# Kernel optimization log

Hardware: AMD Instinct MI355X
Metric: run time of the kernel (lower is better)

Reference implementation:

```python
import jax, jax.numpy as jnp
import numpy as np

LEAK = 0.1
LOG_2PI = float(np.log(2.0 * np.pi))


def setup_inputs() -> dict:
    key = jax.random.key(0)
    k1, k2, k3, k4 = jax.random.split(key, 4)
    B, S, K = 128, 8192, 16
    obvs = jax.random.normal(k1, (B, S, 1), dtype=jnp.float32)
    mu = jax.random.normal(k2, (K,), dtype=jnp.float32)
    log_sigma = 0.1 * jax.random.normal(k3, (K,), dtype=jnp.float32)
    prior_logits = jax.random.normal(k4, (K,), dtype=jnp.float32)
    return {"obvs": obvs, "mu": mu, "log_sigma": log_sigma, "prior_logits": prior_logits}


def _log_transition(num_states: int) -> jnp.ndarray:
    # LeakyTransfer: diagonal-dominant stochastic matrix, stay prob 1-leak,
    # leak mass spread uniformly over the other K-1 states.
    eye = jnp.eye(num_states, dtype=jnp.float32)
    A = (1.0 - LEAK) * eye + (LEAK / (num_states - 1)) * (1.0 - eye)
    return jnp.log(A)


def reference(obvs, mu, log_sigma, prior_logits):
    K = mu.shape[0]
    # Gaussian emission NLL per state: [B, S, K]
    sigma = jnp.exp(log_sigma)
    nll = 0.5 * ((obvs - mu) / sigma) ** 2 + log_sigma + 0.5 * LOG_2PI
    ln_em = -nll  # ln_emission_probs

    log_prior = jax.nn.log_softmax(prior_logits)  # CategoricalPrior
    logA = _log_transition(K)  # [K, K] (from -> to)

    # forward recursion: carry[b, j] = ln_em[b, t, j] + logsumexp_i(carry[b, i] + logA[i, j])
    init = ln_em[:, 0, :] + log_prior  # [B, K]
    em_rest = jnp.swapaxes(ln_em[:, 1:, :], 0, 1)  # [S-1, B, K]

    def step(carry, em_t):
        trans = jax.nn.logsumexp(carry[:, :, None] + logA[None, :, :], axis=1)  # [B, K]
        carry = em_t + trans
        return carry, None

    final, _ = jax.lax.scan(step, init, em_rest)
    return jnp.sum(jax.nn.logsumexp(final, axis=-1))
```

## Files before the change

### kernel.cpp

```cpp
#include <hip/hip_runtime.h>

#define NB 128
#define NS 8192
#define NC 128
#define NCP 8
#define NL (NS / NC)
#define M4 (NL / 4)

#define LOG2E 1.4426950408889634f
#define HLOG2PI 0.918938533204672742f
#define LN2 0.69314718055994531f

#define ROWS 20
#define UNIT 640
#define SLOT 320

typedef float v2f __attribute__((ext_vector_type(2)));

__device__ __forceinline__ float fexp2(float x) { return __builtin_amdgcn_exp2f(x); }
__device__ __forceinline__ float flog2(float x) { return __builtin_amdgcn_logf(x); }

__device__ __forceinline__ float gsum16(float v) {
    v += __shfl_xor(v, 1, 16);
    v += __shfl_xor(v, 2, 16);
    v += __shfl_xor(v, 4, 16);
    v += __shfl_xor(v, 8, 16);
    return v;
}
__device__ __forceinline__ float gmax16(float v) {
    v = fmaxf(v, __shfl_xor(v, 1, 16));
    v = fmaxf(v, __shfl_xor(v, 2, 16));
    v = fmaxf(v, __shfl_xor(v, 4, 16));
    v = fmaxf(v, __shfl_xor(v, 8, 16));
    return v;
}

template <int K>
__device__ __forceinline__ int rotk(int x) {
    return __builtin_amdgcn_mov_dpp(x, 0x120 + K, 0xF, 0xF, true);
}

__device__ __forceinline__ float step2(v2f (&Wv)[8], float T, float xx,
                                       float A2, float B2, float C2) {
    const float amb = 0.9f - 0.1f / 15.0f;
    const float bco = 0.1f / 15.0f;
    float myl = fexp2(fmaf(xx, fmaf(xx, A2, B2), C2));
    int mi = __float_as_int(myl);
    float bT = bco * T;
    v2f bT2 = {bT, bT};
    v2f amb2 = {amb, amb};
    v2f L0 = {myl,                          __int_as_float(rotk<1>(mi))};
    v2f L1 = {__int_as_float(rotk<2>(mi)),  __int_as_float(rotk<3>(mi))};
    v2f L2 = {__int_as_float(rotk<4>(mi)),  __int_as_float(rotk<5>(mi))};
    v2f L3 = {__int_as_float(rotk<6>(mi)),  __int_as_float(rotk<7>(mi))};
    v2f L4 = {__int_as_float(rotk<8>(mi)),  __int_as_float(rotk<9>(mi))};
    v2f L5 = {__int_as_float(rotk<10>(mi)), __int_as_float(rotk<11>(mi))};
    v2f L6 = {__int_as_float(rotk<12>(mi)), __int_as_float(rotk<13>(mi))};
    v2f L7 = {__int_as_float(rotk<14>(mi)), __int_as_float(rotk<15>(mi))};
    Wv[0] = __builtin_elementwise_fma(amb2, Wv[0], bT2) * L0;
    Wv[1] = __builtin_elementwise_fma(amb2, Wv[1], bT2) * L1;
    Wv[2] = __builtin_elementwise_fma(amb2, Wv[2], bT2) * L2;
    Wv[3] = __builtin_elementwise_fma(amb2, Wv[3], bT2) * L3;
    Wv[4] = __builtin_elementwise_fma(amb2, Wv[4], bT2) * L4;
    Wv[5] = __builtin_elementwise_fma(amb2, Wv[5], bT2) * L5;
    Wv[6] = __builtin_elementwise_fma(amb2, Wv[6], bT2) * L6;
    Wv[7] = __builtin_elementwise_fma(amb2, Wv[7], bT2) * L7;
    v2f s = ((Wv[0] + Wv[1]) + (Wv[2] + Wv[3])) + ((Wv[4] + Wv[5]) + (Wv[6] + Wv[7]));
    return s.x + s.y;
}

__device__ __forceinline__ void combineUnits(float* lds, int ua, int ub, int ud, int lane) {
    const float* MbR = lds + ub * UNIT;
    const float* MaT = lds + ua * UNIT + SLOT;
    float mxa = lds[ua * UNIT + 16];
    float mxb = lds[ub * UNIT + 16];
    int a = lane >> 3, cc = lane & 7;
    float b0[16], b1[16], a0[16], a1[16];
    const float4* pb0 = (const float4*)(MbR + (2 * a) * ROWS);
    const float4* pb1 = (const float4*)(MbR + (2 * a + 1) * ROWS);
    const float4* pa0 = (const float4*)(MaT + (2 * cc) * ROWS);
    const float4* pa1 = (const float4*)(MaT + (2 * cc + 1) * ROWS);
#pragma unroll
    for (int q = 0; q < 4; ++q) {
        *(float4*)&b0[4 * q] = pb0[q];
        *(float4*)&b1[4 * q] = pb1[q];
        *(float4*)&a0[4 * q] = pa0[q];
        *(float4*)&a1[4 * q] = pa1[q];
    }
    float c00 = 0.f, c01 = 0.f, c10 = 0.f, c11 = 0.f;
#pragma unroll
    for (int k = 0; k < 16; ++k) {
        c00 = fmaf(b0[k], a0[k], c00);
        c01 = fmaf(b0[k], a1[k], c01);
        c10 = fmaf(b1[k], a0[k], c10);
        c11 = fmaf(b1[k], a1[k], c11);
    }
    float cs0 = c00 + c10;
    float cs1 = c01 + c11;
    cs0 += __shfl_xor(cs0, 8);  cs1 += __shfl_xor(cs1, 8);
    cs0 += __shfl_xor(cs0, 16); cs1 += __shfl_xor(cs1, 16);
    cs0 += __shfl_xor(cs0, 32); cs1 += __shfl_xor(cs1, 32);
    float mxc = fmaxf(cs0, cs1);
    mxc = fmaxf(mxc, __shfl_xor(mxc, 1));
    mxc = fmaxf(mxc, __shfl_xor(mxc, 2));
    mxc = fmaxf(mxc, __shfl_xor(mxc, 4));
    float is = 1.0f / mxc;
    c00 *= is; c01 *= is; c10 *= is; c11 *= is;
    float* dR = lds + ud * UNIT;
    float* dT = lds + ud * UNIT + SLOT;
    *(float2*)(dR + (2 * a) * ROWS + 2 * cc)     = make_float2(c00, c01);
    *(float2*)(dR + (2 * a + 1) * ROWS + 2 * cc) = make_float2(c10, c11);
    *(float2*)(dT + (2 * cc) * ROWS + 2 * a)     = make_float2(c00, c10);
    *(float2*)(dT + (2 * cc + 1) * ROWS + 2 * a) = make_float2(c01, c11);
    if (lane == 0) lds[ud * UNIT + 16] = mxa + mxb + flog2(mxc);
}

__global__ __launch_bounds__(256, 4) void hmm_phase1(const float* __restrict__ obvs,
                                                     const float* __restrict__ mu,
                                                     const float* __restrict__ log_sigma,
                                                     float* __restrict__ wsW,
                                                     float* __restrict__ wsM,
                                                     float* __restrict__ out) {
    __shared__ float lds[16 * UNIT];
    int tid = blockIdx.x * 256 + threadIdx.x;
    if (tid == 0) out[0] = 0.0f;
    int r = threadIdx.x & 15;
    int u = threadIdx.x >> 4;
    int g = tid >> 4;
    int b = g >> 7;
    int c = g & (NC - 1);

    float ls = log_sigma[r];
    float mk = mu[r];
    float iv = fexp2(-2.0f * LOG2E * ls);
    float A2 = -0.5f * LOG2E * iv;
    float B2 = LOG2E * mk * iv;
    float C2 = LOG2E * (-0.5f * mk * mk * iv - ls - HLOG2PI);

    v2f Wv[8];
#pragma unroll
    for (int i = 0; i < 8; ++i) Wv[i] = (v2f){0.0f, 0.0f};
    Wv[0].x = 1.0f;
    int ilog = 0;
    float T = 1.0f;

    const float4* ob4 = (const float4*)(obvs + (long)b * NS) + c * M4;
    float4 xv = ob4[0];
    float4 xn = ob4[1];
    if (c) T = step2(Wv, T, xv.x, A2, B2, C2);
    T = step2(Wv, T, xv.y, A2, B2, C2);
    T = step2(Wv, T, xv.z, A2, B2, C2);
    T = step2(Wv, T, xv.w, A2, B2, C2);
    {
        int te = (__float_as_int(T) >> 23) & 255;
        int ok = (te != 0);
        float s = ok ? __int_as_float((254 - te) << 23) : 1.0f;
        ilog += ok ? (te - 127) : 0;
        v2f s2 = {s, s};
#pragma unroll
        for (int i = 0; i < 8; ++i) Wv[i] *= s2;
        T *= s;
    }
    xv = xn;
    for (int m = 1; m < M4; ++m) {
        xn = ob4[(m + 1) < M4 ? (m + 1) : m];
        T = step2(Wv, T, xv.x, A2, B2, C2);
        T = step2(Wv, T, xv.y, A2, B2, C2);
        T = step2(Wv, T, xv.z, A2, B2, C2);
        T = step2(Wv, T, xv.w, A2, B2, C2);
        int te = (__float_as_int(T) >> 23) & 255;
        int ok = (te != 0);
        float s = ok ? __int_as_float((254 - te) << 23) : 1.0f;
        ilog += ok ? (te - 127) : 0;
        v2f s2 = {s, s};
#pragma unroll
        for (int i = 0; i < 8; ++i) Wv[i] *= s2;
        T *= s;
        xv = xn;
    }

    int sid[16];
    sid[0] = r;
    sid[1]  = rotk<1>(r);   sid[2]  = rotk<2>(r);   sid[3]  = rotk<3>(r);
    sid[4]  = rotk<4>(r);   sid[5]  = rotk<5>(r);   sid[6]  = rotk<6>(r);
    sid[7]  = rotk<7>(r);   sid[8]  = rotk<8>(r);   sid[9]  = rotk<9>(r);
    sid[10] = rotk<10>(r);  sid[11] = rotk<11>(r);  sid[12] = rotk<12>(r);
    sid[13] = rotk<13>(r);  sid[14] = rotk<14>(r);  sid[15] = rotk<15>(r);

    float lg = (float)ilog + flog2(T);
    float mx = gmax16(lg);
    float sc = fexp2((float)ilog - mx);

    float* Ru = lds + u * UNIT;
    float* Tu = lds + u * UNIT + SLOT;
#pragma unroll
    for (int i = 0; i < 8; ++i) {
        float w0 = Wv[i].x * sc;
        float w1 = Wv[i].y * sc;
        int j0 = sid[2 * i], j1 = sid[2 * i + 1];
        Ru[j0 * ROWS + r] = w0;
        Ru[j1 * ROWS + r] = w1;
        Tu[r * ROWS + j0] = w0;
        Tu[r * ROWS + j1] = w1;
    }
    if (r == 0) Ru[16] = mx;
    __syncthreads();

    int lane = threadIdx.x & 63;
    int wid = threadIdx.x >> 6;
#pragma unroll
    for (int q = 0; q < 2; ++q) {
        int p = 2 * wid + q;
        combineUnits(lds, 2 * p, 2 * p + 1, 2 * p, lane);
    }
    __syncthreads();
    if (wid < 4) combineUnits(lds, 4 * wid, 4 * wid + 2, 4 * wid, lane);
    __syncthreads();
    if (wid < 2) combineUnits(lds, 8 * wid, 8 * wid + 4, 8 * wid, lane);
    __syncthreads();
    if (wid == 0) combineUnits(lds, 0, 8, 0, lane);
    __syncthreads();

    wsW[(long)blockIdx.x * 256 + threadIdx.x] =
        lds[(threadIdx.x >> 4) * ROWS + (threadIdx.x & 15)];
    if (threadIdx.x == 0) wsM[blockIdx.x] = lds[16];
}

__device__ __forceinline__ void mat16_mul(float* dR, float* dT,
                                          const float* MbR, const float* MaT,
                                          int lane) {
    int a = lane >> 3;
    int cc = lane & 7;
    float b0[16], b1[16], a0[16], a1[16];
    const float4* pb0 = (const float4*)(MbR + (2 * a) * ROWS);
    const float4* pb1 = (const float4*)(MbR + (2 * a + 1) * ROWS);
    const float4* pa0 = (const float4*)(MaT + (2 * cc) * ROWS);
    const float4* pa1 = (const float4*)(MaT + (2 * cc + 1) * ROWS);
#pragma unroll
    for (int q = 0; q < 4; ++q) {
        *(float4*)&b0[4 * q] = pb0[q];
        *(float4*)&b1[4 * q] = pb1[q];
        *(float4*)&a0[4 * q] = pa0[q];
        *(float4*)&a1[4 * q] = pa1[q];
    }
    float c00 = 0.f, c01 = 0.f, c10 = 0.f, c11 = 0.f;
#pragma unroll
    for (int k = 0; k < 16; ++k) {
        c00 = fmaf(b0[k], a0[k], c00);
        c01 = fmaf(b0[k], a1[k], c01);
        c10 = fmaf(b1[k], a0[k], c10);
        c11 = fmaf(b1[k], a1[k], c11);
    }
    *(float2*)(dR + (2 * a) * ROWS + 2 * cc)     = make_float2(c00, c01);
    *(float2*)(dR + (2 * a + 1) * ROWS + 2 * cc) = make_float2(c10, c11);
    if (dT) {
        *(float2*)(dT + (2 * cc) * ROWS + 2 * a)     = make_float2(c00, c10);
        *(float2*)(dT + (2 * cc + 1) * ROWS + 2 * a) = make_float2(c01, c11);
    }
}

__global__ __launch_bounds__(256, 2) void hmm_phase23(const float* __restrict__ obvs,
                                                      const float* __restrict__ mu,
                                                      const float* __restrict__ log_sigma,
                                                      const float* __restrict__ prior_logits,
                                                      const float* __restrict__ wsW,
                                                      const float* __restrict__ wsM,
                                                      float* __restrict__ out) {
    __shared__ float smem[10560];
    float* stage = smem;
    float* scr   = smem + 5120;
    float* resB  = smem + 10240;

    int bb = blockIdx.x;
    int tid = threadIdx.x;
    int wid = tid >> 6;
    int lane = tid & 63;

    const float4* src = (const float4*)(wsW + (long)bb * NCP * 256);
#pragma unroll
    for (int q = 0; q < 2; ++q) {
        int f = tid + q * 256;
        float4 v = src[f];
        int m = f >> 6, idx = f & 63, j = idx >> 2, kq = idx & 3;
        *(float4*)(stage + m * UNIT + j * ROWS + kq * 4) = v;
        float* Tb = stage + m * UNIT + SLOT;
        Tb[(4 * kq + 0) * ROWS + j] = v.x;
        Tb[(4 * kq + 1) * ROWS + j] = v.y;
        Tb[(4 * kq + 2) * ROWS + j] = v.z;
        Tb[(4 * kq + 3) * ROWS + j] = v.w;
    }
    __syncthreads();
    if (wid < 4)
        mat16_mul(scr + wid * UNIT, scr + wid * UNIT + SLOT,
                  stage + (2 * wid + 1) * UNIT, stage + (2 * wid) * UNIT + SLOT, lane);
    __syncthreads();
    if (wid < 2)
        mat16_mul(scr + (4 + wid) * UNIT, scr + (4 + wid) * UNIT + SLOT,
                  scr + (2 * wid + 1) * UNIT, scr + (2 * wid) * UNIT + SLOT, lane);
    __syncthreads();
    if (wid == 0)
        mat16_mul(resB, nullptr, scr + 5 * UNIT, scr + 4 * UNIT + SLOT, lane);
    __syncthreads();

    if (tid < 16) {
        int jj = tid;
        float ls = log_sigma[jj];
        float mk = mu[jj];
        float iv = fexp2(-2.0f * LOG2E * ls);
        float A2 = -0.5f * LOG2E * iv;
        float B2 = LOG2E * mk * iv;
        float C2 = LOG2E * (-0.5f * mk * mk * iv - ls - HLOG2PI);
        float x = obvs[(long)bb * NS];
        float e = fexp2(LOG2E * prior_logits[jj]);
        float Z = gsum16(e);
        float p0 = fexp2(fmaf(x, fmaf(x, A2, B2), C2)) * e;
        const float* Mrow = resB + jj * ROWS;
        float mr[16];
        *(float4*)&mr[0]  = ((const float4*)Mrow)[0];
        *(float4*)&mr[4]  = ((const float4*)Mrow)[1];
        *(float4*)&mr[8]  = ((const float4*)Mrow)[2];
        *(float4*)&mr[12] = ((const float4*)Mrow)[3];
        float q = 0.0f;
#pragma unroll
        for (int rr = 0; rr < 16; ++rr) q = fmaf(mr[rr], __shfl(p0, rr, 16), q);
        float Tq = gsum16(q);
        float pm = (jj < NCP) ? wsM[bb * NCP + jj] : 0.0f;
        float msum = gsum16(pm);
        if (jj == 0) {
            float res = (flog2(Tq) - flog2(Z) + msum) * LN2;
            atomicAdd(out, res);
        }
    }
}

extern "C" void kernel_launch(void* const* d_in, const int* in_sizes, int n_in,
                              void* d_out, int out_size, void* d_ws, size_t ws_size,
                              hipStream_t stream) {
    const float* obvs = (const float*)d_in[0];
    const float* mu = (const float*)d_in[1];
    const float* log_sigma = (const float*)d_in[2];
    const float* prior_logits = (const float*)d_in[3];
    float* out = (float*)d_out;

    float* wsW = (float*)d_ws;
    float* wsM = wsW + (size_t)NB * NCP * 256;

    hmm_phase1<<<dim3(NB * NC * 16 / 256), dim3(256), 0, stream>>>(obvs, mu, log_sigma,
                                                                   wsW, wsM, out);
    hmm_phase23<<<dim3(NB), dim3(256), 0, stream>>>(obvs, mu, log_sigma, prior_logits,
                                                    wsW, wsM, out);
}
```

Baseline: 92.77 us.

## Double sequence chunks per batch and drop transposed LDS copies in combine

Splits each sequence into twice as many chunks, so each phase-1 thread group runs half as many serial forward steps and the grid doubles. The transposed matrix copy in LDS is removed: combine now reads rows of A directly with float2 loads, which halves LDS per block and lets the occupancy hint rise to 6. Phase 2/3 now reduces 16 chunk matrices per batch with the normalized combineUnits tree instead of the unnormalized mat16_mul, and adds the accumulated log-scale term to the result. In exchange, more partial matrices are written to and read from the workspace, and more combine work is done per batch.

```diff
diff --git a/kernel.cpp b/kernel.cpp
--- a/kernel.cpp
+++ b/kernel.cpp
@@ -2,8 +2,8 @@
 
 #define NB 128
 #define NS 8192
-#define NC 128
-#define NCP 8
+#define NC 256
+#define NCP 16
 #define NL (NS / NC)
 #define M4 (NL / 4)
 
@@ -12,8 +12,7 @@
 #define LN2 0.69314718055994531f
 
 #define ROWS 20
-#define UNIT 640
-#define SLOT 320
+#define UNIT 320
 
 typedef float v2f __attribute__((ext_vector_type(2)));
 
@@ -71,29 +70,26 @@
 
 __device__ __forceinline__ void combineUnits(float* lds, int ua, int ub, int ud, int lane) {
     const float* MbR = lds + ub * UNIT;
-    const float* MaT = lds + ua * UNIT + SLOT;
+    const float* MaR = lds + ua * UNIT;
     float mxa = lds[ua * UNIT + 16];
     float mxb = lds[ub * UNIT + 16];
     int a = lane >> 3, cc = lane & 7;
-    float b0[16], b1[16], a0[16], a1[16];
+    float b0[16], b1[16];
     const float4* pb0 = (const float4*)(MbR + (2 * a) * ROWS);
     const float4* pb1 = (const float4*)(MbR + (2 * a + 1) * ROWS);
-    const float4* pa0 = (const float4*)(MaT + (2 * cc) * ROWS);
-    const float4* pa1 = (const float4*)(MaT + (2 * cc + 1) * ROWS);
 #pragma unroll
     for (int q = 0; q < 4; ++q) {
         *(float4*)&b0[4 * q] = pb0[q];
         *(float4*)&b1[4 * q] = pb1[q];
-        *(float4*)&a0[4 * q] = pa0[q];
-        *(float4*)&a1[4 * q] = pa1[q];
     }
     float c00 = 0.f, c01 = 0.f, c10 = 0.f, c11 = 0.f;
 #pragma unroll
     for (int k = 0; k < 16; ++k) {
-        c00 = fmaf(b0[k], a0[k], c00);
-        c01 = fmaf(b0[k], a1[k], c01);
-        c10 = fmaf(b1[k], a0[k], c10);
-        c11 = fmaf(b1[k], a1[k], c11);
+        float2 av = *(const float2*)(MaR + k * ROWS + 2 * cc);
+        c00 = fmaf(b0[k], av.x, c00);
+        c01 = fmaf(b0[k], av.y, c01);
+        c10 = fmaf(b1[k], av.x, c10);
+        c11 = fmaf(b1[k], av.y, c11);
     }
     float cs0 = c00 + c10;
     float cs1 = c01 + c11;
@@ -107,15 +103,12 @@
     float is = 1.0f / mxc;
     c00 *= is; c01 *= is; c10 *= is; c11 *= is;
     float* dR = lds + ud * UNIT;
-    float* dT = lds + ud * UNIT + SLOT;
     *(float2*)(dR + (2 * a) * ROWS + 2 * cc)     = make_float2(c00, c01);
     *(float2*)(dR + (2 * a + 1) * ROWS + 2 * cc) = make_float2(c10, c11);
-    *(float2*)(dT + (2 * cc) * ROWS + 2 * a)     = make_float2(c00, c10);
-    *(float2*)(dT + (2 * cc + 1) * ROWS + 2 * a) = make_float2(c01, c11);
     if (lane == 0) lds[ud * UNIT + 16] = mxa + mxb + flog2(mxc);
 }
 
-__global__ __launch_bounds__(256, 4) void hmm_phase1(const float* __restrict__ obvs,
+__global__ __launch_bounds__(256, 6) void hmm_phase1(const float* __restrict__ obvs,
                                                      const float* __restrict__ mu,
                                                      const float* __restrict__ log_sigma,
                                                      float* __restrict__ wsW,
@@ -127,7 +120,7 @@
     int r = threadIdx.x & 15;
     int u = threadIdx.x >> 4;
     int g = tid >> 4;
-    int b = g >> 7;
+    int b = g >> 8;
     int c = g & (NC - 1);
 
     float ls = log_sigma[r];
@@ -179,29 +172,17 @@
         xv = xn;
     }
 
-    int sid[16];
-    sid[0] = r;
-    sid[1]  = rotk<1>(r);   sid[2]  = rotk<2>(r);   sid[3]  = rotk<3>(r);
-    sid[4]  = rotk<4>(r);   sid[5]  = rotk<5>(r);   sid[6]  = rotk<6>(r);
-    sid[7]  = rotk<7>(r);   sid[8]  = rotk<8>(r);   sid[9]  = rotk<9>(r);
-    sid[10] = rotk<10>(r);  sid[11] = rotk<11>(r);  sid[12] = rotk<12>(r);
-    sid[13] = rotk<13>(r);  sid[14] = rotk<14>(r);  sid[15] = rotk<15>(r);
-
     float lg = (float)ilog + flog2(T);
     float mx = gmax16(lg);
     float sc = fexp2((float)ilog - mx);
 
     float* Ru = lds + u * UNIT;
-    float* Tu = lds + u * UNIT + SLOT;
 #pragma unroll
     for (int i = 0; i < 8; ++i) {
-        float w0 = Wv[i].x * sc;
-        float w1 = Wv[i].y * sc;
-        int j0 = sid[2 * i], j1 = sid[2 * i + 1];
-        Ru[j0 * ROWS + r] = w0;
-        Ru[j1 * ROWS + r] = w1;
-        Tu[r * ROWS + j0] = w0;
-        Tu[r * ROWS + j1] = w1;
+        int j0 = (r + 2 * i) & 15;
+        int j1 = (r + 2 * i + 1) & 15;
+        Ru[j0 * ROWS + r] = Wv[i].x * sc;
+        Ru[j1 * ROWS + r] = Wv[i].y * sc;
     }
     if (r == 0) Ru[16] = mx;
     __syncthreads();
@@ -224,39 +205,6 @@
     wsW[(long)blockIdx.x * 256 + threadIdx.x] =
         lds[(threadIdx.x >> 4) * ROWS + (threadIdx.x & 15)];
     if (threadIdx.x == 0) wsM[blockIdx.x] = lds[16];
-}
-
-__device__ __forceinline__ void mat16_mul(float* dR, float* dT,
-                                          const float* MbR, const float* MaT,
-                                          int lane) {
-    int a = lane >> 3;
-    int cc = lane & 7;
-    float b0[16], b1[16], a0[16], a1[16];
-    const float4* pb0 = (const float4*)(MbR + (2 * a) * ROWS);
-    const float4* pb1 = (const float4*)(MbR + (2 * a + 1) * ROWS);
-    const float4* pa0 = (const float4*)(MaT + (2 * cc) * ROWS);
-    const float4* pa1 = (const float4*)(MaT + (2 * cc + 1) * ROWS);
-#pragma unroll
-    for (int q = 0; q < 4; ++q) {
-        *(float4*)&b0[4 * q] = pb0[q];
-        *(float4*)&b1[4 * q] = pb1[q];
-        *(float4*)&a0[4 * q] = pa0[q];
-        *(float4*)&a1[4 * q] = pa1[q];
-    }
-    float c00 = 0.f, c01 = 0.f, c10 = 0.f, c11 = 0.f;
-#pragma unroll
-    for (int k = 0; k < 16; ++k) {
-        c00 = fmaf(b0[k], a0[k], c00);
-        c01 = fmaf(b0[k], a1[k], c01);
-        c10 = fmaf(b1[k], a0[k], c10);
-        c11 = fmaf(b1[k], a1[k], c11);
-    }
-    *(float2*)(dR + (2 * a) * ROWS + 2 * cc)     = make_float2(c00, c01);
-    *(float2*)(dR + (2 * a + 1) * ROWS + 2 * cc) = make_float2(c10, c11);
-    if (dT) {
-        *(float2*)(dT + (2 * cc) * ROWS + 2 * a)     = make_float2(c00, c10);
-        *(float2*)(dT + (2 * cc + 1) * ROWS + 2 * a) = make_float2(c01, c11);
-    }
 }
 
 __global__ __launch_bounds__(256, 2) void hmm_phase23(const float* __restrict__ obvs,
@@ -266,11 +214,7 @@
                                                       const float* __restrict__ wsW,
                                                       const float* __restrict__ wsM,
                                                       float* __restrict__ out) {
-    __shared__ float smem[10560];
-    float* stage = smem;
-    float* scr   = smem + 5120;
-    float* resB  = smem + 10240;
-
+    __shared__ float lds[16 * UNIT];
     int bb = blockIdx.x;
     int tid = threadIdx.x;
     int wid = tid >> 6;
@@ -278,28 +222,26 @@
 
     const float4* src = (const float4*)(wsW + (long)bb * NCP * 256);
 #pragma unroll
-    for (int q = 0; q < 2; ++q) {
+    for (int q = 0; q < 4; ++q) {
         int f = tid + q * 256;
         float4 v = src[f];
         int m = f >> 6, idx = f & 63, j = idx >> 2, kq = idx & 3;
-        *(float4*)(stage + m * UNIT + j * ROWS + kq * 4) = v;
-        float* Tb = stage + m * UNIT + SLOT;
-        Tb[(4 * kq + 0) * ROWS + j] = v.x;
-        Tb[(4 * kq + 1) * ROWS + j] = v.y;
-        Tb[(4 * kq + 2) * ROWS + j] = v.z;
-        Tb[(4 * kq + 3) * ROWS + j] = v.w;
-    }
-    __syncthreads();
-    if (wid < 4)
-        mat16_mul(scr + wid * UNIT, scr + wid * UNIT + SLOT,
-                  stage + (2 * wid + 1) * UNIT, stage + (2 * wid) * UNIT + SLOT, lane);
-    __syncthreads();
-    if (wid < 2)
-        mat16_mul(scr + (4 + wid) * UNIT, scr + (4 + wid) * UNIT + SLOT,
-                  scr + (2 * wid + 1) * UNIT, scr + (2 * wid) * UNIT + SLOT, lane);
-    __syncthreads();
-    if (wid == 0)
-        mat16_mul(resB, nullptr, scr + 5 * UNIT, scr + 4 * UNIT + SLOT, lane);
+        *(float4*)(lds + m * UNIT + j * ROWS + kq * 4) = v;
+    }
+    if (tid < 16) lds[tid * UNIT + 16] = 0.0f;
+    __syncthreads();
+
+#pragma unroll
+    for (int q = 0; q < 2; ++q) {
+        int p = 2 * wid + q;
+        combineUnits(lds, 2 * p, 2 * p + 1, 2 * p, lane);
+    }
+    __syncthreads();
+    if (wid < 4) combineUnits(lds, 4 * wid, 4 * wid + 2, 4 * wid, lane);
+    __syncthreads();
+    if (wid < 2) combineUnits(lds, 8 * wid, 8 * wid + 4, 8 * wid, lane);
+    __syncthreads();
+    if (wid == 0) combineUnits(lds, 0, 8, 0, lane);
     __syncthreads();
 
     if (tid < 16) {
@@ -314,7 +256,7 @@
         float e = fexp2(LOG2E * prior_logits[jj]);
         float Z = gsum16(e);
         float p0 = fexp2(fmaf(x, fmaf(x, A2, B2), C2)) * e;
-        const float* Mrow = resB + jj * ROWS;
+        const float* Mrow = lds + jj * ROWS;
         float mr[16];
         *(float4*)&mr[0]  = ((const float4*)Mrow)[0];
         *(float4*)&mr[4]  = ((const float4*)Mrow)[1];
@@ -324,10 +266,10 @@
 #pragma unroll
         for (int rr = 0; rr < 16; ++rr) q = fmaf(mr[rr], __shfl(p0, rr, 16), q);
         float Tq = gsum16(q);
-        float pm = (jj < NCP) ? wsM[bb * NCP + jj] : 0.0f;
+        float pm = wsM[bb * NCP + jj];
         float msum = gsum16(pm);
         if (jj == 0) {
-            float res = (flog2(Tq) - flog2(Z) + msum) * LN2;
+            float res = (flog2(Tq) + lds[16] - flog2(Z) + msum) * LN2;
             atomicAdd(out, res);
         }
     }
```

Result: slower. 95.80 us (+3.3%).
